# Performance work log

Measured on AMD Instinct MI355X. Metric: run time of the kernel, lower is better.

## Reference

```python
import jax, jax.numpy as jnp
import numpy as np

B, N, D, K = 128, 1000, 196, 48
SIGMA = 0.05


def setup_inputs() -> dict:
    key = jax.random.key(0)
    kx, kn = jax.random.split(key)
    x = jax.random.normal(kx, (B, D), dtype=jnp.float32)
    noise = jax.random.normal(kn, (B, N, D), dtype=jnp.float32)
    return {"x": x, "noise": noise, "sigma": SIGMA}


def reference(x, noise, sigma):
    # x: (b, d); noise: (b, n, d)
    b, d = x.shape
    n = noise.shape[1]
    perturbed = x[:, None, :] + noise * sigma          # (b, n, d)
    _, idx = jax.lax.top_k(perturbed, K)               # (b, n, k) indices into d
    idx = jnp.sort(idx, axis=-1)                       # sorted, as in torch code
    # indicators[b,k,d'] = mean_n one_hot(idx[b,n,k])[d']
    # computed via scatter-add, avoiding the (b,n,k,d) one-hot tensor
    b_idx = jnp.arange(b)[:, None, None]               # (b,1,1)
    k_idx = jnp.arange(K)[None, None, :]               # (1,1,k)
    indicators = jnp.zeros((b, K, d), dtype=x.dtype).at[b_idx, k_idx, idx].add(1.0 / n)
    return indicators
```

## Files before the change

### kernel.cpp

```cpp
#include <hip/hip_runtime.h>


#define BB 128
#define NN 1000
#define DD 196
#define KK 48

constexpr int SPLIT   = 8;
constexpr int ROWS    = NN / SPLIT;
constexpr int THREADS = 256;
constexpr int NWAVES  = THREADS / 64;
constexpr int DH      = DD / 2;
constexpr int LDSN    = KK * DH;

__device__ __forceinline__ unsigned key_of(float v) {
  unsigned u = __float_as_uint(v);
  return u ^ (0x80000000u | (unsigned)((int)u >> 31));
}

__device__ __forceinline__ int mbcnt64(unsigned long long m) {
  return __builtin_amdgcn_mbcnt_hi((unsigned)(m >> 32),
         __builtin_amdgcn_mbcnt_lo((unsigned)m, 0));
}

__global__ __launch_bounds__(THREADS) void ptopk_kernel(
    const float* __restrict__ x, const float* __restrict__ noise,
    const float* __restrict__ sigp, float* __restrict__ out) {
  __shared__ unsigned cnt[LDSN];
  const int tid   = threadIdx.x;
  const int b     = blockIdx.x / SPLIT;
  const int split = blockIdx.x % SPLIT;

  for (int i = tid; i < LDSN; i += THREADS) cnt[i] = 0u;
  __syncthreads();

  const float sigma = sigp[0];
  const int lane = tid & 63;
  const int wv   = tid >> 6;
  const bool lv  = lane < 49;

  float4 xv = make_float4(0.f, 0.f, 0.f, 0.f);
  if (lv) xv = *reinterpret_cast<const float4*>(x + b * DD + 4 * lane);
  unsigned xk0 = lv ? key_of(xv.x) : 0u;
  unsigned xk1 = lv ? key_of(xv.y) : 0u;
  unsigned xk2 = lv ? key_of(xv.z) : 0u;
  unsigned xk3 = lv ? key_of(xv.w) : 0u;

  unsigned piv = 0u;
  #pragma unroll
  for (int bit = 31; bit >= 0; --bit) {
    unsigned cand = piv | (1u << bit);
    int c = __popcll(__ballot(xk0 >= cand)) + __popcll(__ballot(xk1 >= cand))
          + __popcll(__ballot(xk2 >= cand)) + __popcll(__ballot(xk3 >= cand));
    if (c >= KK) piv = cand;
  }

  const float* nbase = noise + ((size_t)b * NN + (size_t)split * ROWS) * DD;

  for (int r = wv; r < ROWS; r += NWAVES) {
    float4 nv = make_float4(0.f, 0.f, 0.f, 0.f);
    if (lv) nv = *reinterpret_cast<const float4*>(nbase + (size_t)r * DD + 4 * lane);
    const unsigned k0 = lv ? key_of(fmaf(sigma, nv.x, xv.x)) : 0u;
    const unsigned k1 = lv ? key_of(fmaf(sigma, nv.y, xv.y)) : 0u;
    const unsigned k2 = lv ? key_of(fmaf(sigma, nv.z, xv.z)) : 0u;
    const unsigned k3 = lv ? key_of(fmaf(sigma, nv.w, xv.w)) : 0u;

    const int c = __popcll(__ballot(k0 > piv)) + __popcll(__ballot(k1 > piv))
                + __popcll(__ballot(k2 > piv)) + __popcll(__ballot(k3 > piv));

    unsigned T = 0u;
    if (c >= KK) {
      int rem = c - (KK - 1);
      unsigned m0 = (k0 > piv) ? k0 : 0xFFFFFFFFu;
      unsigned m1 = (k1 > piv) ? k1 : 0xFFFFFFFFu;
      unsigned m2 = (k2 > piv) ? k2 : 0xFFFFFFFFu;
      unsigned m3 = (k3 > piv) ? k3 : 0xFFFFFFFFu;
      for (;;) {
        unsigned mm = min(min(m0, m1), min(m2, m3));
        #pragma unroll
        for (int off = 32; off >= 1; off >>= 1)
          mm = min(mm, (unsigned)__shfl_xor((int)mm, off, 64));
        int cv = __popcll(__ballot(m0 == mm)) + __popcll(__ballot(m1 == mm))
               + __popcll(__ballot(m2 == mm)) + __popcll(__ballot(m3 == mm));
        if (cv >= rem) { T = mm; break; }
        rem -= cv;
        m0 = (m0 == mm) ? 0xFFFFFFFFu : m0;
        m1 = (m1 == mm) ? 0xFFFFFFFFu : m1;
        m2 = (m2 == mm) ? 0xFFFFFFFFu : m2;
        m3 = (m3 == mm) ? 0xFFFFFFFFu : m3;
      }
    } else {
      int rem = KK - c;
      unsigned m0 = (k0 <= piv) ? k0 : 0u;
      unsigned m1 = (k1 <= piv) ? k1 : 0u;
      unsigned m2 = (k2 <= piv) ? k2 : 0u;
      unsigned m3 = (k3 <= piv) ? k3 : 0u;
      for (;;) {
        unsigned mm = max(max(m0, m1), max(m2, m3));
        #pragma unroll
        for (int off = 32; off >= 1; off >>= 1)
          mm = max(mm, (unsigned)__shfl_xor((int)mm, off, 64));
        int cv = __popcll(__ballot(m0 == mm)) + __popcll(__ballot(m1 == mm))
               + __popcll(__ballot(m2 == mm)) + __popcll(__ballot(m3 == mm));
        if (cv >= rem) { T = mm; break; }
        rem -= cv;
        m0 = (m0 == mm) ? 0u : m0;
        m1 = (m1 == mm) ? 0u : m1;
        m2 = (m2 == mm) ? 0u : m2;
        m3 = (m3 == mm) ? 0u : m3;
      }
    }

    const unsigned long long e0 = __ballot(k0 == T), e1 = __ballot(k1 == T),
                             e2 = __ballot(k2 == T), e3 = __ballot(k3 == T);
    const int cnt_gt = __popcll(__ballot(k0 > T)) + __popcll(__ballot(k1 > T))
                     + __popcll(__ballot(k2 > T)) + __popcll(__ballot(k3 > T));
    const int budget = KK - cnt_gt;
    const bool eq0 = (k0 == T), eq1 = (k1 == T), eq2 = (k2 == T), eq3 = (k3 == T);
    int tr = mbcnt64(e0) + mbcnt64(e1) + mbcnt64(e2) + mbcnt64(e3);
    const bool s0 = (k0 > T) || (eq0 && tr < budget); tr += eq0 ? 1 : 0;
    const bool s1 = (k1 > T) || (eq1 && tr < budget); tr += eq1 ? 1 : 0;
    const bool s2 = (k2 > T) || (eq2 && tr < budget); tr += eq2 ? 1 : 0;
    const bool s3 = (k3 > T) || (eq3 && tr < budget);

    const unsigned long long S0 = __ballot(s0), S1 = __ballot(s1),
                             S2 = __ballot(s2), S3 = __ballot(s3);
    int kp = mbcnt64(S0) + mbcnt64(S1) + mbcnt64(S2) + mbcnt64(S3);
    const int b2 = 2 * lane;
    if (s0) atomicAdd(&cnt[kp * DH + b2],     1u);        kp += s0 ? 1 : 0;
    if (s1) atomicAdd(&cnt[kp * DH + b2],     0x10000u);  kp += s1 ? 1 : 0;
    if (s2) atomicAdd(&cnt[kp * DH + b2 + 1], 1u);        kp += s2 ? 1 : 0;
    if (s3) atomicAdd(&cnt[kp * DH + b2 + 1], 0x10000u);
  }

  __syncthreads();

  const float invn = 1.0f / (float)NN;
  float* ob = out + (size_t)b * KK * DD;
  for (int i = tid; i < LDSN; i += THREADS) {
    const unsigned cv = cnt[i];
    if (cv) {
      const int k   = i / DH;
      const int dd2 = i - k * DH;
      const unsigned lo = cv & 0xFFFFu, hi = cv >> 16;
      float* p = ob + k * DD + 2 * dd2;
      if (lo) atomicAdd(p,     (float)lo * invn);
      if (hi) atomicAdd(p + 1, (float)hi * invn);
    }
  }
}

extern "C" void kernel_launch(void* const* d_in, const int* in_sizes, int n_in,
                              void* d_out, int out_size, void* d_ws, size_t ws_size,
                              hipStream_t stream) {
  (void)in_sizes; (void)n_in; (void)d_ws; (void)ws_size;
  const float* x     = (const float*)d_in[0];
  const float* noise = (const float*)d_in[1];
  const float* sig   = (const float*)d_in[2];
  float* out = (float*)d_out;

  hipMemsetAsync(d_out, 0, (size_t)out_size * sizeof(float), stream);
  ptopk_kernel<<<dim3(BB * SPLIT), dim3(THREADS), 0, stream>>>(x, noise, sig, out);
}
```

Before: 192.4 us.

## Hoist pivot search into separate kernel, prefetch noise rows, use swizzle reductions

```diff
diff --git a/kernel.cpp b/kernel.cpp
--- a/kernel.cpp
+++ b/kernel.cpp
@@ -8,7 +8,7 @@
 
 constexpr int SPLIT   = 8;
 constexpr int ROWS    = NN / SPLIT;
-constexpr int THREADS = 256;
+constexpr int THREADS = 512;
 constexpr int NWAVES  = THREADS / 64;
 constexpr int DH      = DD / 2;
 constexpr int LDSN    = KK * DH;
@@ -23,47 +23,88 @@
          __builtin_amdgcn_mbcnt_lo((unsigned)m, 0));
 }
 
-__global__ __launch_bounds__(THREADS) void ptopk_kernel(
-    const float* __restrict__ x, const float* __restrict__ noise,
-    const float* __restrict__ sigp, float* __restrict__ out) {
-  __shared__ unsigned cnt[LDSN];
-  const int tid   = threadIdx.x;
-  const int b     = blockIdx.x / SPLIT;
-  const int split = blockIdx.x % SPLIT;
-
-  for (int i = tid; i < LDSN; i += THREADS) cnt[i] = 0u;
-  __syncthreads();
-
-  const float sigma = sigp[0];
-  const int lane = tid & 63;
-  const int wv   = tid >> 6;
+__device__ __forceinline__ unsigned wave_min_u32(unsigned m) {
+  unsigned mm = m;
+  mm = min(mm, (unsigned)__builtin_amdgcn_ds_swizzle((int)mm, 0x041F));
+  mm = min(mm, (unsigned)__builtin_amdgcn_ds_swizzle((int)mm, 0x081F));
+  mm = min(mm, (unsigned)__builtin_amdgcn_ds_swizzle((int)mm, 0x101F));
+  mm = min(mm, (unsigned)__builtin_amdgcn_ds_swizzle((int)mm, 0x201F));
+  mm = min(mm, (unsigned)__builtin_amdgcn_ds_swizzle((int)mm, 0x401F));
+  unsigned a = (unsigned)__builtin_amdgcn_readlane((int)mm, 0);
+  unsigned b = (unsigned)__builtin_amdgcn_readlane((int)mm, 32);
+  return min(a, b);
+}
+
+__device__ __forceinline__ unsigned wave_max_u32(unsigned m) {
+  unsigned mm = m;
+  mm = max(mm, (unsigned)__builtin_amdgcn_ds_swizzle((int)mm, 0x041F));
+  mm = max(mm, (unsigned)__builtin_amdgcn_ds_swizzle((int)mm, 0x081F));
+  mm = max(mm, (unsigned)__builtin_amdgcn_ds_swizzle((int)mm, 0x101F));
+  mm = max(mm, (unsigned)__builtin_amdgcn_ds_swizzle((int)mm, 0x201F));
+  mm = max(mm, (unsigned)__builtin_amdgcn_ds_swizzle((int)mm, 0x401F));
+  unsigned a = (unsigned)__builtin_amdgcn_readlane((int)mm, 0);
+  unsigned b = (unsigned)__builtin_amdgcn_readlane((int)mm, 32);
+  return max(a, b);
+}
+
+__global__ __launch_bounds__(64) void pivot_kernel(
+    const float* __restrict__ x, unsigned* __restrict__ piv) {
+  const int b    = blockIdx.x;
+  const int lane = threadIdx.x;
   const bool lv  = lane < 49;
-
   float4 xv = make_float4(0.f, 0.f, 0.f, 0.f);
   if (lv) xv = *reinterpret_cast<const float4*>(x + b * DD + 4 * lane);
   unsigned xk0 = lv ? key_of(xv.x) : 0u;
   unsigned xk1 = lv ? key_of(xv.y) : 0u;
   unsigned xk2 = lv ? key_of(xv.z) : 0u;
   unsigned xk3 = lv ? key_of(xv.w) : 0u;
-
-  unsigned piv = 0u;
+  unsigned p = 0u;
   #pragma unroll
   for (int bit = 31; bit >= 0; --bit) {
-    unsigned cand = piv | (1u << bit);
+    unsigned cand = p | (1u << bit);
     int c = __popcll(__ballot(xk0 >= cand)) + __popcll(__ballot(xk1 >= cand))
           + __popcll(__ballot(xk2 >= cand)) + __popcll(__ballot(xk3 >= cand));
-    if (c >= KK) piv = cand;
+    if (c >= KK) p = cand;
   }
+  if (lane == 0) piv[b] = p;
+}
+
+__global__ __launch_bounds__(THREADS) void ptopk_kernel(
+    const float* __restrict__ x, const float* __restrict__ noise,
+    const float* __restrict__ sigp, const unsigned* __restrict__ pivp,
+    float* __restrict__ out) {
+  __shared__ unsigned cnt[LDSN];
+  const int tid   = threadIdx.x;
+  const int b     = blockIdx.x / SPLIT;
+  const int split = blockIdx.x % SPLIT;
+
+  for (int i = tid; i < LDSN; i += THREADS) cnt[i] = 0u;
+  __syncthreads();
+
+  const float sigma  = sigp[0];
+  const unsigned piv = pivp[b];
+  const int lane = tid & 63;
+  const int wv   = tid >> 6;
+  const bool lv  = lane < 49;
+
+  float4 xv = make_float4(0.f, 0.f, 0.f, 0.f);
+  if (lv) xv = *reinterpret_cast<const float4*>(x + b * DD + 4 * lane);
 
   const float* nbase = noise + ((size_t)b * NN + (size_t)split * ROWS) * DD;
 
+  float4 nv = make_float4(0.f, 0.f, 0.f, 0.f);
+  if (lv && wv < ROWS)
+    nv = *reinterpret_cast<const float4*>(nbase + (size_t)wv * DD + 4 * lane);
+
   for (int r = wv; r < ROWS; r += NWAVES) {
-    float4 nv = make_float4(0.f, 0.f, 0.f, 0.f);
-    if (lv) nv = *reinterpret_cast<const float4*>(nbase + (size_t)r * DD + 4 * lane);
-    const unsigned k0 = lv ? key_of(fmaf(sigma, nv.x, xv.x)) : 0u;
-    const unsigned k1 = lv ? key_of(fmaf(sigma, nv.y, xv.y)) : 0u;
-    const unsigned k2 = lv ? key_of(fmaf(sigma, nv.z, xv.z)) : 0u;
-    const unsigned k3 = lv ? key_of(fmaf(sigma, nv.w, xv.w)) : 0u;
+    const float4 cur = nv;
+    if (lv && (r + NWAVES) < ROWS)
+      nv = *reinterpret_cast<const float4*>(nbase + (size_t)(r + NWAVES) * DD + 4 * lane);
+
+    const unsigned k0 = lv ? key_of(fmaf(sigma, cur.x, xv.x)) : 0u;
+    const unsigned k1 = lv ? key_of(fmaf(sigma, cur.y, xv.y)) : 0u;
+    const unsigned k2 = lv ? key_of(fmaf(sigma, cur.z, xv.z)) : 0u;
+    const unsigned k3 = lv ? key_of(fmaf(sigma, cur.w, xv.w)) : 0u;
 
     const int c = __popcll(__ballot(k0 > piv)) + __popcll(__ballot(k1 > piv))
                 + __popcll(__ballot(k2 > piv)) + __popcll(__ballot(k3 > piv));
@@ -76,10 +117,7 @@
       unsigned m2 = (k2 > piv) ? k2 : 0xFFFFFFFFu;
       unsigned m3 = (k3 > piv) ? k3 : 0xFFFFFFFFu;
       for (;;) {
-        unsigned mm = min(min(m0, m1), min(m2, m3));
-        #pragma unroll
-        for (int off = 32; off >= 1; off >>= 1)
-          mm = min(mm, (unsigned)__shfl_xor((int)mm, off, 64));
+        const unsigned mm = wave_min_u32(min(min(m0, m1), min(m2, m3)));
         int cv = __popcll(__ballot(m0 == mm)) + __popcll(__ballot(m1 == mm))
                + __popcll(__ballot(m2 == mm)) + __popcll(__ballot(m3 == mm));
         if (cv >= rem) { T = mm; break; }
@@ -96,10 +134,7 @@
       unsigned m2 = (k2 <= piv) ? k2 : 0u;
       unsigned m3 = (k3 <= piv) ? k3 : 0u;
       for (;;) {
-        unsigned mm = max(max(m0, m1), max(m2, m3));
-        #pragma unroll
-        for (int off = 32; off >= 1; off >>= 1)
-          mm = max(mm, (unsigned)__shfl_xor((int)mm, off, 64));
+        const unsigned mm = wave_max_u32(max(max(m0, m1), max(m2, m3)));
         int cv = __popcll(__ballot(m0 == mm)) + __popcll(__ballot(m1 == mm))
                + __popcll(__ballot(m2 == mm)) + __popcll(__ballot(m3 == mm));
         if (cv >= rem) { T = mm; break; }
@@ -153,12 +188,14 @@
 extern "C" void kernel_launch(void* const* d_in, const int* in_sizes, int n_in,
                               void* d_out, int out_size, void* d_ws, size_t ws_size,
                               hipStream_t stream) {
-  (void)in_sizes; (void)n_in; (void)d_ws; (void)ws_size;
+  (void)in_sizes; (void)n_in; (void)ws_size;
   const float* x     = (const float*)d_in[0];
   const float* noise = (const float*)d_in[1];
   const float* sig   = (const float*)d_in[2];
   float* out = (float*)d_out;
+  unsigned* piv = (unsigned*)d_ws;
 
   hipMemsetAsync(d_out, 0, (size_t)out_size * sizeof(float), stream);
-  ptopk_kernel<<<dim3(BB * SPLIT), dim3(THREADS), 0, stream>>>(x, noise, sig, out);
-}
+  pivot_kernel<<<dim3(BB), dim3(64), 0, stream>>>(x, piv);
+  ptopk_kernel<<<dim3(BB * SPLIT), dim3(THREADS), 0, stream>>>(x, noise, sig, piv, out);
+}
```

Result: faster. 168.8 us (-12.3%).
